# Kernel tuning notes

Measured on AMD Instinct MI355X. Metric: run time of the kernel, lower is better.

Reference implementation:

```python
import jax, jax.numpy as jnp
import numpy as np

B, C, T, H, W = 1, 512, 4, 32, 32
NUM_HEADS = 8
HEAD_DIM = C // NUM_HEADS


def setup_inputs() -> dict:
    key = jax.random.key(0)
    k1, k2, k3 = jax.random.split(key, 3)
    x = jax.random.normal(k1, (B, C, T, H, W), dtype=jnp.float32)
    w_qkv = jax.random.normal(k2, (3 * C, C), dtype=jnp.float32) * (1.0 / np.sqrt(C))
    w_out = jax.random.normal(k3, (C, C), dtype=jnp.float32) * (1.0 / np.sqrt(C))
    b_out = jnp.zeros((C,), dtype=jnp.float32)
    return {"x": x, "w_qkv": w_qkv, "w_out": w_out, "b_out": b_out}


def reference(x, w_qkv, w_out, b_out):
    b, c, t, h, w = x.shape
    n = t * h * w
    nh, hd = NUM_HEADS, c // NUM_HEADS
    x_flat = x.reshape(b, c, n)                      # [B,C,N]
    # 1x1 Conv3d == pointwise channel GEMM
    qkv = jnp.einsum('oc,bcn->bon', w_qkv, x_flat)   # [B,3C,N]
    q, k, v = jnp.split(qkv, 3, axis=1)
    q = q.reshape(b, nh, hd, n)
    k = k.reshape(b, nh, hd, n)
    v = v.reshape(b, nh, hd, n)
    dots = jnp.einsum('bhdi,bhdj->bhij', q, k) * (hd ** -0.5)  # [B,h,N,N]
    attn = jax.nn.softmax(dots, axis=-1)
    out = jnp.einsum('bhij,bhdj->bhdi', attn, v)     # [B,h,d,N]
    out = out.reshape(b, c, n)
    out = jnp.einsum('oc,bcn->bon', w_out, out) + b_out[None, :, None]
    return out.reshape(b, c, t, h, w) + x
```

## Files before the change

### kernel.cpp

```cpp
#include <hip/hip_runtime.h>
#include <hip/hip_bf16.h>


#define N_TOK 4096
#define C_DIM 512
#define NH    8
#define HD    64

#define QSCALE  0.18033688011112042f

typedef __bf16 bf16x8 __attribute__((ext_vector_type(8)));
typedef float f32x4 __attribute__((ext_vector_type(4)));

__device__ __forceinline__ f32x4 mfma16(bf16x8 a, bf16x8 b, f32x4 c) {
    return __builtin_amdgcn_mfma_f32_16x16x32_bf16(a, b, c, 0, 0, 0);
}

__device__ __forceinline__ bool probe_f32(const unsigned short* x) {
    int lane = threadIdx.x & 63;
    int hits = 0;
    #pragma unroll
    for (int r = 0; r < 4; r++) {
        unsigned short u = x[(lane * 4 + r) * 2];
        hits += (((u >> 7) & 0xFF) >= 140) ? 1 : 0;
    }
    #pragma unroll
    for (int off = 1; off < 64; off <<= 1) hits += __shfl_xor(hits, off);
    return hits >= 8;
}

__global__ __launch_bounds__(256) void prepare(
    const void* __restrict__ xv, const void* __restrict__ wq,
    const void* __restrict__ wo, const void* __restrict__ bo,
    __hip_bfloat16* __restrict__ xt, __hip_bfloat16* __restrict__ wqc,
    __hip_bfloat16* __restrict__ woc, __hip_bfloat16* __restrict__ bc)
{
    bool f32 = probe_f32((const unsigned short*)xv);
    int b = blockIdx.x, tid = threadIdx.x;
    if (b < 512) {
        __shared__ __hip_bfloat16 t[64][68];
        int n0 = (b & 63) * 64, c0 = (b >> 6) * 64;
        int nl = tid & 15, cl = tid >> 4;
        #pragma unroll
        for (int p = 0; p < 4; p++) {
            int c = cl + p * 16;
            ushort4 pk;
            if (f32) {
                float4 v = *reinterpret_cast<const float4*>(
                    (const float*)xv + (size_t)(c0 + c) * N_TOK + n0 + nl * 4);
                union { unsigned short u; __hip_bfloat16 h; } a0, a1, a2, a3;
                a0.h = __float2bfloat16(v.x); a1.h = __float2bfloat16(v.y);
                a2.h = __float2bfloat16(v.z); a3.h = __float2bfloat16(v.w);
                pk.x = a0.u; pk.y = a1.u; pk.z = a2.u; pk.w = a3.u;
            } else {
                pk = *reinterpret_cast<const ushort4*>(
                    (const __hip_bfloat16*)xv + (size_t)(c0 + c) * N_TOK + n0 + nl * 4);
            }
            *reinterpret_cast<ushort4*>(&t[c][nl * 4]) = pk;
        }
        __syncthreads();
        int cc = tid & 15, nr = tid >> 4;
        #pragma unroll
        for (int p = 0; p < 4; p++) {
            int n = nr + p * 16;
            ushort4 v;
            v.x = *reinterpret_cast<unsigned short*>(&t[cc * 4 + 0][n]);
            v.y = *reinterpret_cast<unsigned short*>(&t[cc * 4 + 1][n]);
            v.z = *reinterpret_cast<unsigned short*>(&t[cc * 4 + 2][n]);
            v.w = *reinterpret_cast<unsigned short*>(&t[cc * 4 + 3][n]);
            *reinterpret_cast<ushort4*>(xt + (size_t)(n0 + n) * C_DIM + c0 + cc * 4) = v;
        }
    } else {
        const int N1 = 3 * C_DIM * C_DIM, N2 = C_DIM * C_DIM, N3 = C_DIM;
        int total4 = (N1 + N2 + N3) >> 2;
        int stride = 128 * 256;
        for (int g = (b - 512) * 256 + tid; g < total4; g += stride) {
            int i = g * 4;
            const void* src; __hip_bfloat16* dst; int j;
            if (i < N1)           { src = wq; dst = wqc; j = i; }
            else if (i < N1 + N2) { src = wo; dst = woc; j = i - N1; }
            else                  { src = bo; dst = bc;  j = i - N1 - N2; }
            ushort4 pk;
            if (f32) {
                float4 v = *reinterpret_cast<const float4*>((const float*)src + j);
                union { unsigned short u; __hip_bfloat16 h; } a0, a1, a2, a3;
                a0.h = __float2bfloat16(v.x); a1.h = __float2bfloat16(v.y);
                a2.h = __float2bfloat16(v.z); a3.h = __float2bfloat16(v.w);
                pk.x = a0.u; pk.y = a1.u; pk.z = a2.u; pk.w = a3.u;
            } else {
                pk = *reinterpret_cast<const ushort4*>((const __hip_bfloat16*)src + j);
            }
            *reinterpret_cast<ushort4*>(dst + j) = pk;
        }
    }
}

__global__ __launch_bounds__(128) void qkv_gemm(
    const __hip_bfloat16* __restrict__ w,
    const __hip_bfloat16* __restrict__ xt,
    __hip_bfloat16* __restrict__ qt,
    unsigned char* __restrict__ kvg)
{
    __shared__ alignas(16) unsigned char sx[2][16384];
    __shared__ alignas(16) unsigned char swt[2][8192];
    int tid = threadIdx.x, lane = tid & 63, wv = tid >> 6;
    int l15 = lane & 15, quad = lane >> 4;
    int n0b = blockIdx.x * 128;
    int n0w = n0b + wv * 64;
    int m0w = blockIdx.y * 64;
    int rl = lane >> 3, cs = lane & 7;

    f32x4 acc[4][4] = {};

    auto stageF = [&](int c, int buf) {
        #pragma unroll
        for (int k = 0; k < 8; k++) {
            int g = wv * 8 + k;
            int row = g * 8 + rl;
            const unsigned char* src = (const unsigned char*)xt
                + (size_t)(n0b + row) * 1024 + c * 128 + ((cs ^ (row & 7)) << 4);
            __builtin_amdgcn_global_load_lds(
                (const __attribute__((address_space(1))) void*)src,
                (__attribute__((address_space(3))) void*)(&sx[buf][g * 1024]),
                16, 0, 0);
        }
        #pragma unroll
        for (int k = 0; k < 4; k++) {
            int g = wv * 4 + k;
            int row = g * 8 + rl;
            const unsigned char* src = (const unsigned char*)w
                + (size_t)(m0w + row) * 1024 + c * 128 + ((cs ^ (row & 7)) << 4);
            __builtin_amdgcn_global_load_lds(
                (const __attribute__((address_space(1))) void*)src,
                (__attribute__((address_space(3))) void*)(&swt[buf][g * 1024]),
                16, 0, 0);
        }
    };

    auto compute = [&](int buf) {
        bf16x8 af[2][4], bfr[2][4];
        #pragma unroll
        for (int hf = 0; hf < 2; hf++) {
            #pragma unroll
            for (int i = 0; i < 4; i++) {
                int row = wv * 64 + i * 16 + l15;
                af[hf][i] = *reinterpret_cast<const bf16x8*>(
                    &sx[buf][row * 128 + (((hf * 4 + quad) ^ (row & 7)) << 4)]);
            }
            #pragma unroll
            for (int j = 0; j < 4; j++) {
                int row = j * 16 + l15;
                bfr[hf][j] = *reinterpret_cast<const bf16x8*>(
                    &swt[buf][row * 128 + (((hf * 4 + quad) ^ (row & 7)) << 4)]);
            }
        }
        #pragma unroll
        for (int hf = 0; hf < 2; hf++)
            #pragma unroll
            for (int i = 0; i < 4; i++)
                #pragma unroll
                for (int j = 0; j < 4; j++)
                    acc[i][j] = mfma16(af[hf][i], bfr[hf][j], acc[i][j]);
    };

    stageF(0, 0);
    #pragma unroll
    for (int c = 0; c < 8; c++) {
        if (c + 1 < 8) stageF(c + 1, (c + 1) & 1);
        if (c + 1 < 8) asm volatile("s_waitcnt vmcnt(12)" ::: "memory");
        else           asm volatile("s_waitcnt vmcnt(0)" ::: "memory");
        __builtin_amdgcn_s_barrier();
        __builtin_amdgcn_sched_barrier(0);
        compute(c & 1);
        asm volatile("" ::: "memory");
        __builtin_amdgcn_s_barrier();
    }

    int kind = m0w >> 9;
    int h = (m0w >> 6) & 7;
    int jb = n0w >> 6;
    unsigned char* sb = &sx[0][wv * 8192];
    #pragma unroll
    for (int i = 0; i < 4; i++)
        #pragma unroll
        for (int j = 0; j < 4; j++)
            #pragma unroll
            for (int r = 0; r < 4; r++) {
                int nn = i * 16 + quad * 4 + r;
                int dd = j * 16 + l15;
                float v = acc[i][j][r];
                int row, cg, byo;
                if (kind == 0)      { row = nn; cg = dd >> 3;              byo = (dd & 7) * 2; v *= QSCALE; }
                else if (kind == 1) { row = nn; cg = (dd >> 3) ^ (nn & 7); byo = (dd & 7) * 2; }
                else {
                    row = dd;
                    int cc = ((nn >> 5) << 2) | ((nn >> 2) & 3);
                    cg = cc ^ (dd & 7);
                    byo = ((nn >> 4) & 1) * 8 + (nn & 3) * 2;
                }
                int phys = cg ^ ((row >> 1) & 7);
                *reinterpret_cast<__hip_bfloat16*>(sb + row * 128 + phys * 16 + byo)
                    = __float2bfloat16(v);
            }
    unsigned char* gbase;
    if (kind == 0) gbase = (unsigned char*)(qt + ((size_t)h * N_TOK + n0w) * HD);
    else           gbase = kvg + (((size_t)h * 64 + jb) << 14) + (kind == 2 ? 8192 : 0);
    #pragma unroll
    for (int it = 0; it < 8; it++) {
        int idx = it * 64 + lane;
        int row = idx >> 3, phys = (idx & 7) ^ ((idx >> 4) & 7);
        uint4 val = *reinterpret_cast<const uint4*>(sb + row * 128 + phys * 16);
        *reinterpret_cast<uint4*>(gbase + idx * 16) = val;
    }
}

__global__ __launch_bounds__(256) void attn_kernel(
    const __hip_bfloat16* __restrict__ qt,
    const unsigned char* __restrict__ kv,
    __hip_bfloat16* __restrict__ Opart,
    float* __restrict__ lpart,
    __hip_bfloat16* __restrict__ ot,
    int tbase, int trem)
{
    __shared__ alignas(16) unsigned char kvb[4][16384];
    int tid = threadIdx.x, lane = tid & 63, wv = tid >> 6;
    int l15 = lane & 15, quad = lane >> 4;
    int s7 = l15 & 7;
    int h = blockIdx.x >> 4;
    int i0 = (blockIdx.x & 15) * 256 + wv * 64;
    int kslice = blockIdx.y;
    const unsigned char* kvh = kv + ((size_t)h << 20);

    int jt0 = kslice * tbase + min(kslice, trem);
    int ntile = tbase + (kslice < trem ? 1 : 0);

    bf16x8 qB[4][2];
    #pragma unroll
    for (int g = 0; g < 4; g++)
        #pragma unroll
        for (int hf = 0; hf < 2; hf++)
            qB[g][hf] = *reinterpret_cast<const bf16x8*>(
                qt + (h * N_TOK + i0 + g * 16 + l15) * HD + hf * 32 + quad * 8);

    bf16x8 vones;
    #pragma unroll
    for (int i = 0; i < 8; i++) vones[i] = (__bf16)1.0f;

    f32x4 oacc[4][4] = {};
    f32x4 lsum[4] = {};

    int koff[2], vo[2];
    #pragma unroll
    for (int hf = 0; hf < 2; hf++)
        koff[hf] = l15 * 128 + (((hf * 4 + quad) ^ s7) << 4);
    #pragma unroll
    for (int p = 0; p < 2; p++)
        vo[p] = l15 * 128 + (((p * 4 + quad) ^ s7) << 4);

    auto stage = [&](int jb, int buf) {
        const unsigned char* s = kvh + ((size_t)jb << 14) + wv * 4096 + lane * 16;
        unsigned char* d = &kvb[buf][0] + wv * 4096;
        #pragma unroll
        for (int it = 0; it < 4; it++)
            __builtin_amdgcn_global_load_lds(
                (const __attribute__((address_space(1))) void*)(s + it * 1024),
                (__attribute__((address_space(3))) void*)(d + it * 1024),
                16, 0, 0);
    };

    auto body = [&](const unsigned char* kb) {
        const unsigned char* vb = kb + 8192;
        bf16x8 kf[8];
        #pragma unroll
        for (int nt = 0; nt < 4; nt++)
            #pragma unroll
            for (int hf = 0; hf < 2; hf++)
                kf[nt * 2 + hf] = *reinterpret_cast<const bf16x8*>(kb + nt * 2048 + koff[hf]);
        bf16x8 vf[4][2];
        #pragma unroll
        for (int db = 0; db < 4; db++)
            #pragma unroll
            for (int p = 0; p < 2; p++)
                vf[db][p] = *reinterpret_cast<const bf16x8*>(vb + db * 2048 + vo[p]);

        f32x4 sA[4], sB[4];
        #pragma unroll
        for (int nt = 0; nt < 4; nt++) {
            f32x4 z = {};
            z = mfma16(kf[nt * 2], qB[0][0], z);
            sA[nt] = mfma16(kf[nt * 2 + 1], qB[0][1], z);
        }
        #pragma unroll
        for (int g = 0; g < 4; g++) {
            f32x4* scur = (g & 1) ? sB : sA;
            f32x4* snxt = (g & 1) ? sA : sB;
            if (g < 3) {
                #pragma unroll
                for (int nt = 0; nt < 4; nt++) {
                    f32x4 z = {};
                    z = mfma16(kf[nt * 2], qB[g + 1][0], z);
                    snxt[nt] = mfma16(kf[nt * 2 + 1], qB[g + 1][1], z);
                }
            }
            bf16x8 pf[2];
            #pragma unroll
            for (int p = 0; p < 2; p++)
                #pragma unroll
                for (int i = 0; i < 4; i++) {
                    pf[p][i]     = (__bf16)__builtin_amdgcn_exp2f(scur[p * 2][i]);
                    pf[p][i + 4] = (__bf16)__builtin_amdgcn_exp2f(scur[p * 2 + 1][i]);
                }
            #pragma unroll
            for (int p = 0; p < 2; p++) {
                #pragma unroll
                for (int db = 0; db < 4; db++)
                    oacc[g][db] = mfma16(pf[p], vf[db][p], oacc[g][db]);
                lsum[g] = mfma16(pf[p], vones, lsum[g]);
            }
        }
    };

    stage(jt0, 0);
    if (ntile > 1) stage(jt0 + 1, 1);
    if (ntile > 2) stage(jt0 + 2, 2);
    for (int t = 0; t < ntile; t++) {
        if (t + 2 < ntile)      asm volatile("s_waitcnt vmcnt(8)" ::: "memory");
        else if (t + 1 < ntile) asm volatile("s_waitcnt vmcnt(4)" ::: "memory");
        else                    asm volatile("s_waitcnt vmcnt(0)" ::: "memory");
        __builtin_amdgcn_s_barrier();
        __builtin_amdgcn_sched_barrier(0);
        if (t + 3 < ntile) stage(jt0 + t + 3, (t + 3) & 3);
        body(&kvb[t & 3][0]);
    }

    if (Opart) {
        __hip_bfloat16* Ob = Opart + (size_t)kslice * (NH * N_TOK * HD);
        float* lb = lpart + (size_t)kslice * (NH * N_TOK);
        #pragma unroll
        for (int g = 0; g < 4; g++) {
            #pragma unroll
            for (int db = 0; db < 4; db++)
                #pragma unroll
                for (int r = 0; r < 4; r++) {
                    int i = i0 + g * 16 + quad * 4 + r;
                    Ob[(h * N_TOK + i) * HD + db * 16 + l15] =
                        __float2bfloat16(oacc[g][db][r]);
                }
            if (l15 == 0)
                #pragma unroll
                for (int r = 0; r < 4; r++)
                    lb[h * N_TOK + i0 + g * 16 + quad * 4 + r] = lsum[g][r];
        }
    } else {
        #pragma unroll
        for (int g = 0; g < 4; g++)
            #pragma unroll
            for (int db = 0; db < 4; db++)
                #pragma unroll
                for (int r = 0; r < 4; r++) {
                    int i = i0 + g * 16 + quad * 4 + r;
                    ot[i * C_DIM + h * HD + db * 16 + l15] =
                        __float2bfloat16(oacc[g][db][r] / lsum[g][r]);
                }
    }
}

__global__ __launch_bounds__(256) void combine_kernel(
    const __hip_bfloat16* __restrict__ Opart, const float* __restrict__ lpart,
    __hip_bfloat16* __restrict__ ot, int splitk)
{
    int tid = blockIdx.x * 256 + threadIdx.x;
    int h = tid >> 16, rem = tid & 65535;
    int q = rem >> 4, d4 = rem & 15;
    size_t off = ((size_t)(h * N_TOK + q) * HD) + d4 * 4;
    float o[4] = {};
    float l = 0.f;
    for (int k = 0; k < splitk; k++) {
        ushort4 u = *reinterpret_cast<const ushort4*>(
            Opart + (size_t)k * (NH * N_TOK * HD) + off);
        union { unsigned short us; __hip_bfloat16 h; } c0, c1, c2, c3;
        c0.us = u.x; c1.us = u.y; c2.us = u.z; c3.us = u.w;
        o[0] += __bfloat162float(c0.h); o[1] += __bfloat162float(c1.h);
        o[2] += __bfloat162float(c2.h); o[3] += __bfloat162float(c3.h);
        l += lpart[k * (NH * N_TOK) + h * N_TOK + q];
    }
    float inv = 1.0f / l;
    union { unsigned long long u; __hip_bfloat16 b[4]; } pk;
    #pragma unroll
    for (int i = 0; i < 4; i++) pk.b[i] = __float2bfloat16(o[i] * inv);
    *reinterpret_cast<unsigned long long*>(ot + q * C_DIM + h * HD + d4 * 4) = pk.u;
}

__global__ __launch_bounds__(256) void proj_gemm(
    const __hip_bfloat16* __restrict__ w,
    const __hip_bfloat16* __restrict__ ot,
    const __hip_bfloat16* __restrict__ bias,
    const void* __restrict__ xv,
    void* __restrict__ outv)
{
    bool f32 = probe_f32((const unsigned short*)xv);
    int tid = threadIdx.x, lane = tid & 63, wv = tid >> 6;
    int l15 = lane & 15, quad = lane >> 4;
    int m0 = blockIdx.y * 32;
    int n0 = blockIdx.x * 128 + wv * 32;
    f32x4 acc[2][2] = {};
    bf16x8 a[4][2], b[4][2];
    #pragma unroll
    for (int pl = 0; pl < 3; pl++) {
        int kn = pl * 32 + quad * 8;
        #pragma unroll
        for (int mt = 0; mt < 2; mt++)
            a[pl][mt] = *reinterpret_cast<const bf16x8*>(w + (m0 + mt * 16 + l15) * 512 + kn);
        #pragma unroll
        for (int nt = 0; nt < 2; nt++)
            b[pl][nt] = *reinterpret_cast<const bf16x8*>(ot + (n0 + nt * 16 + l15) * 512 + kn);
    }
    #pragma unroll
    for (int kk = 0; kk < 16; kk++) {
        int cur = kk & 3;
        if (kk + 3 < 16) {
            int nxt = (kk + 3) & 3;
            int kn = (kk + 3) * 32 + quad * 8;
            #pragma unroll
            for (int mt = 0; mt < 2; mt++)
                a[nxt][mt] = *reinterpret_cast<const bf16x8*>(w + (m0 + mt * 16 + l15) * 512 + kn);
            #pragma unroll
            for (int nt = 0; nt < 2; nt++)
                b[nxt][nt] = *reinterpret_cast<const bf16x8*>(ot + (n0 + nt * 16 + l15) * 512 + kn);
        }
        #pragma unroll
        for (int mt = 0; mt < 2; mt++)
            #pragma unroll
            for (int nt = 0; nt < 2; nt++)
                acc[mt][nt] = mfma16(a[cur][mt], b[cur][nt], acc[mt][nt]);
    }
    #pragma unroll
    for (int mt = 0; mt < 2; mt++)
        #pragma unroll
        for (int nt = 0; nt < 2; nt++)
            #pragma unroll
            for (int r = 0; r < 4; r++) {
                int m = m0 + mt * 16 + quad * 4 + r;
                int n = n0 + nt * 16 + l15;
                int idx = m * N_TOK + n;
                float xr = f32 ? ((const float*)xv)[idx]
                               : __bfloat162float(((const __hip_bfloat16*)xv)[idx]);
                float v = acc[mt][nt][r] + __bfloat162float(bias[m]) + xr;
                if (f32) ((float*)outv)[idx] = v;
                else     ((__hip_bfloat16*)outv)[idx] = __float2bfloat16(v);
            }
}

extern "C" void kernel_launch(void* const* d_in, const int* in_sizes, int n_in,
                              void* d_out, int out_size, void* d_ws, size_t ws_size,
                              hipStream_t stream) {
    const void* x     = d_in[0];
    const void* w_qkv = d_in[1];
    const void* w_out = d_in[2];
    const void* b_out = d_in[3];

    char* ws = (char*)d_ws;
    const size_t MB = 1024 * 1024;
    __hip_bfloat16* xt  = (__hip_bfloat16*)(ws);
    __hip_bfloat16* ot  = (__hip_bfloat16*)(ws);
    __hip_bfloat16* qt  = (__hip_bfloat16*)(ws + 4 * MB);
    unsigned char*  kv  = (unsigned char*) (ws + 8 * MB);
    __hip_bfloat16* wqc = (__hip_bfloat16*)(ws + 16 * MB);
    __hip_bfloat16* woc = (__hip_bfloat16*)(ws + 16 * MB + 0x180000);
    __hip_bfloat16* bc  = (__hip_bfloat16*)(ws + 16 * MB + 0x200000);

    const size_t pbase   = 16 * MB + 0x200800;
    const size_t o_slice = (size_t)NH * N_TOK * HD * 2;
    const size_t l_slice = (size_t)NH * N_TOK * 4;
    int nslice = 1;
    if      (ws_size >= pbase + 4 * (o_slice + l_slice)) nslice = 4;
    else if (ws_size >= pbase + 3 * (o_slice + l_slice)) nslice = 3;
    else if (ws_size >= pbase + 2 * (o_slice + l_slice)) nslice = 2;
    __hip_bfloat16* Opart = (nslice > 1) ? (__hip_bfloat16*)(ws + pbase) : nullptr;
    float* lpart = (nslice > 1) ? (float*)(ws + pbase + (size_t)nslice * o_slice) : nullptr;

    prepare<<<640, 256, 0, stream>>>(x, w_qkv, w_out, b_out, xt, wqc, woc, bc);
    qkv_gemm<<<dim3(32, 24), 128, 0, stream>>>(wqc, xt, qt, kv);

    int tbase = 64 / nslice, trem = 64 % nslice;
    attn_kernel<<<dim3(128, nslice), 256, 0, stream>>>(
        qt, kv, Opart, lpart, ot, tbase, trem);
    if (nslice > 1)
        combine_kernel<<<2048, 256, 0, stream>>>(Opart, lpart, ot, nslice);

    proj_gemm<<<dim3(32, 16), 256, 0, stream>>>(woc, ot, bc, x, d_out);
}
```

Before: 146.9 us.

## Stage output-projection GEMM operands through swizzled LDS with async global-to-LDS loads

```diff
diff --git a/kernel.cpp b/kernel.cpp
--- a/kernel.cpp
+++ b/kernel.cpp
@@ -398,42 +398,81 @@
     const void* __restrict__ xv,
     void* __restrict__ outv)
 {
+    __shared__ alignas(16) unsigned char sot[2][16384];
+    __shared__ alignas(16) unsigned char swt[2][4096];
     bool f32 = probe_f32((const unsigned short*)xv);
     int tid = threadIdx.x, lane = tid & 63, wv = tid >> 6;
     int l15 = lane & 15, quad = lane >> 4;
     int m0 = blockIdx.y * 32;
-    int n0 = blockIdx.x * 128 + wv * 32;
+    int n0b = blockIdx.x * 128;
+    int n0 = n0b + wv * 32;
+    int rl = lane >> 3, cs = lane & 7;
+
     f32x4 acc[2][2] = {};
-    bf16x8 a[4][2], b[4][2];
-    #pragma unroll
-    for (int pl = 0; pl < 3; pl++) {
-        int kn = pl * 32 + quad * 8;
-        #pragma unroll
-        for (int mt = 0; mt < 2; mt++)
-            a[pl][mt] = *reinterpret_cast<const bf16x8*>(w + (m0 + mt * 16 + l15) * 512 + kn);
-        #pragma unroll
-        for (int nt = 0; nt < 2; nt++)
-            b[pl][nt] = *reinterpret_cast<const bf16x8*>(ot + (n0 + nt * 16 + l15) * 512 + kn);
-    }
-    #pragma unroll
-    for (int kk = 0; kk < 16; kk++) {
-        int cur = kk & 3;
-        if (kk + 3 < 16) {
-            int nxt = (kk + 3) & 3;
-            int kn = (kk + 3) * 32 + quad * 8;
+
+    auto stageF = [&](int c, int buf) {
+        #pragma unroll
+        for (int k = 0; k < 4; k++) {
+            int g = wv * 4 + k;
+            int row = g * 8 + rl;
+            const unsigned char* src = (const unsigned char*)ot
+                + (size_t)(n0b + row) * 1024 + c * 128 + ((cs ^ (row & 7)) << 4);
+            __builtin_amdgcn_global_load_lds(
+                (const __attribute__((address_space(1))) void*)src,
+                (__attribute__((address_space(3))) void*)(&sot[buf][g * 1024]),
+                16, 0, 0);
+        }
+        {
+            int g = wv;
+            int row = g * 8 + rl;
+            const unsigned char* src = (const unsigned char*)w
+                + (size_t)(m0 + row) * 1024 + c * 128 + ((cs ^ (row & 7)) << 4);
+            __builtin_amdgcn_global_load_lds(
+                (const __attribute__((address_space(1))) void*)src,
+                (__attribute__((address_space(3))) void*)(&swt[buf][g * 1024]),
+                16, 0, 0);
+        }
+    };
+
+    auto compute = [&](int buf) {
+        bf16x8 af[2][2], bfr[2][2];
+        #pragma unroll
+        for (int hf = 0; hf < 2; hf++) {
+            #pragma unroll
+            for (int mt = 0; mt < 2; mt++) {
+                int row = mt * 16 + l15;
+                af[hf][mt] = *reinterpret_cast<const bf16x8*>(
+                    &swt[buf][row * 128 + (((hf * 4 + quad) ^ (row & 7)) << 4)]);
+            }
+            #pragma unroll
+            for (int nt = 0; nt < 2; nt++) {
+                int row = wv * 32 + nt * 16 + l15;
+                bfr[hf][nt] = *reinterpret_cast<const bf16x8*>(
+                    &sot[buf][row * 128 + (((hf * 4 + quad) ^ (row & 7)) << 4)]);
+            }
+        }
+        #pragma unroll
+        for (int hf = 0; hf < 2; hf++)
             #pragma unroll
             for (int mt = 0; mt < 2; mt++)
-                a[nxt][mt] = *reinterpret_cast<const bf16x8*>(w + (m0 + mt * 16 + l15) * 512 + kn);
-            #pragma unroll
-            for (int nt = 0; nt < 2; nt++)
-                b[nxt][nt] = *reinterpret_cast<const bf16x8*>(ot + (n0 + nt * 16 + l15) * 512 + kn);
-        }
-        #pragma unroll
-        for (int mt = 0; mt < 2; mt++)
-            #pragma unroll
-            for (int nt = 0; nt < 2; nt++)
-                acc[mt][nt] = mfma16(a[cur][mt], b[cur][nt], acc[mt][nt]);
-    }
+                #pragma unroll
+                for (int nt = 0; nt < 2; nt++)
+                    acc[mt][nt] = mfma16(af[hf][mt], bfr[hf][nt], acc[mt][nt]);
+    };
+
+    stageF(0, 0);
+    #pragma unroll
+    for (int c = 0; c < 8; c++) {
+        if (c + 1 < 8) stageF(c + 1, (c + 1) & 1);
+        if (c + 1 < 8) asm volatile("s_waitcnt vmcnt(5)" ::: "memory");
+        else           asm volatile("s_waitcnt vmcnt(0)" ::: "memory");
+        __builtin_amdgcn_s_barrier();
+        __builtin_amdgcn_sched_barrier(0);
+        compute(c & 1);
+        asm volatile("" ::: "memory");
+        __builtin_amdgcn_s_barrier();
+    }
+
     #pragma unroll
     for (int mt = 0; mt < 2; mt++)
         #pragma unroll
```

Measured after the change: 136.0 us (median of 3 runs). 1.08x faster.
